# Kernel tuning notes

Measured on AMD Instinct MI355X. Metric: run time of the kernel, lower is better.

The kernel has to match this reference:

```python
import jax, jax.numpy as jnp
import numpy as np

TEMPERATURE = 0.1
CANTOR_WEIGHT = 0.3
P_POS = 256
GRID = 16
DIM = 512


def _cantor_bias():
    # matches LearnedWormholeRouter._compute_cantor_fingerprints / _compute_cantor_bias
    idx = np.arange(P_POS)
    x = idx % GRID
    y = idx // GRID
    s = x + y
    z = (s * (s + 1) // 2 + y).astype(np.float32)
    fp = z / max(z.max(), 1.0)
    aff = 1.0 - np.abs(fp[None, :] - fp[:, None])
    np.fill_diagonal(aff, -1e9)
    return (aff * CANTOR_WEIGHT).astype(np.float32)


def setup_inputs() -> dict:
    key = jax.random.key(0)
    ks = jax.random.split(key, 8)
    B, P, D = 64, P_POS, DIM
    sc = 0.02
    inp = {
        "x": jax.random.normal(ks[0], (B, P + 1, D), jnp.float32),
        "wq_r": jax.random.normal(ks[1], (D, D), jnp.float32) * sc,
        "bq_r": jnp.zeros((D,), jnp.float32),
        "wk_r": jax.random.normal(ks[2], (D, D), jnp.float32) * sc,
        "bk_r": jnp.zeros((D,), jnp.float32),
        "pos_bias": jnp.asarray(_cantor_bias()),
        "wq": jax.random.normal(ks[3], (D, D), jnp.float32) * sc,
        "bq": jnp.zeros((D,), jnp.float32),
        "wk": jax.random.normal(ks[4], (D, D), jnp.float32) * sc,
        "bk": jnp.zeros((D,), jnp.float32),
        "wv": jax.random.normal(ks[5], (D, D), jnp.float32) * sc,
        "bv": jnp.zeros((D,), jnp.float32),
        "wo": jax.random.normal(ks[6], (D, D), jnp.float32) * sc,
        "bo": jnp.zeros((D,), jnp.float32),
        "num_wormholes": 8,
        "num_heads": 8,
    }
    return inp


def _l2norm(v):
    return v / jnp.sqrt(jnp.sum(v * v, axis=-1, keepdims=True) + 1e-12)


def _gather_wormhole_multihead(xh, routes):
    # xh: [B,H,P,d], routes: [B,P,K] -> [B,H,P,K,d]
    # gather along the position axis, shared routes across heads
    idx = routes[:, None, :, :, None]            # [B,1,P,K,1]
    src = xh[:, :, None, :, :]                   # [B,H,1,P,d]
    return jnp.take_along_axis(src, idx, axis=3)  # [B,H,P,K,d]


def reference(x, wq_r, bq_r, wk_r, bk_r, pos_bias,
              wq, bq, wk, bk, wv, bv, wo, bo,
              num_wormholes, num_heads):
    B, P1, D = x.shape
    P = P1 - 1
    K = num_wormholes
    H = num_heads
    d = D // H

    xp = x[:, 1:, :]  # drop CLS token, [B,P,D]

    # --- LearnedWormholeRouter ---
    q_r = _l2norm(xp @ wq_r + bq_r)
    k_r = _l2norm(xp @ wk_r + bk_r)
    scores = jnp.einsum("bpd,bqd->bpq", q_r, k_r) + pos_bias[None]
    diag = jnp.eye(P, dtype=bool)
    scores = jnp.where(diag[None], -1e9, scores)
    scores_scaled = scores / TEMPERATURE
    topk_scores, routes = jax.lax.top_k(scores_scaled, K)  # [B,P,K]

    # --- wormhole multi-head attention over gathered positions ---
    def heads(w, b):
        return (xp @ w + b).reshape(B, P, H, d).transpose(0, 2, 1, 3)  # [B,H,P,d]

    qh, kh, vh = heads(wq, bq), heads(wk, bk), heads(wv, bv)
    gk = _gather_wormhole_multihead(kh, routes)  # [B,H,P,K,d]
    gv = _gather_wormhole_multihead(vh, routes)  # [B,H,P,K,d]

    att = jnp.einsum("bhpd,bhpkd->bhpk", qh, gk) / jnp.sqrt(jnp.float32(d))
    att = jax.nn.softmax(att, axis=-1)
    ctx = jnp.einsum("bhpk,bhpkd->bhpd", att, gv)
    out = ctx.transpose(0, 2, 1, 3).reshape(B, P, D) @ wo + bo  # [B,P,D]
    return out
```

## Files before the change

kernel.cpp:

```cpp
#include <hip/hip_runtime.h>
#include <math.h>

constexpr int PB = 256;
constexpr int DD = 512;
constexpr int NB = 64;
constexpr int MROWS = NB * PB;

typedef __bf16 bf16x8 __attribute__((ext_vector_type(8)));
typedef float f32x4 __attribute__((ext_vector_type(4)));
typedef unsigned short us8 __attribute__((ext_vector_type(8)));

__device__ __forceinline__ unsigned short f2b(float f) {
  unsigned int u = __float_as_uint(f);
  u += 0x7FFFu + ((u >> 16) & 1u);
  return (unsigned short)(u >> 16);
}
__device__ __forceinline__ float b2f(unsigned short h) {
  return __uint_as_float(((unsigned int)h) << 16);
}

__device__ __forceinline__ void gload16(const void* g, const void* l) {
  __builtin_amdgcn_global_load_lds(
      (const __attribute__((address_space(1))) unsigned int*)(uintptr_t)g,
      (__attribute__((address_space(3))) unsigned int*)(unsigned int)(uintptr_t)l,
      16, 0, 0);
}

__global__ __launch_bounds__(256) void gemm_scores(
    const float* __restrict__ Q, const float* __restrict__ Kr,
    float* __restrict__ S)
{
  __shared__ float As[16][65];
  __shared__ float Bs[16][65];
  const int b = blockIdx.z;
  const int tid = threadIdx.x;
  const int tx = tid & 15, ty = tid >> 4;
  const int p0 = blockIdx.y * 64, q0 = blockIdx.x * 64;
  const float* Qb = Q + (long)b * PB * DD;
  const float* Kb = Kr + (long)b * PB * DD;
  const int a_r = tid >> 2, a_k = (tid & 3) << 2;
  const int b_n = tid & 63, b_k4 = (tid >> 6) << 2;
  float acc[4][4] = {};

  for (int k0 = 0; k0 < DD; k0 += 16) {
    float4 av = *(const float4*)(Qb + (long)(p0 + a_r) * DD + k0 + a_k);
    As[a_k + 0][a_r] = av.x;
    As[a_k + 1][a_r] = av.y;
    As[a_k + 2][a_r] = av.z;
    As[a_k + 3][a_r] = av.w;
    float4 bv = *(const float4*)(Kb + (long)(q0 + b_n) * DD + k0 + b_k4);
    Bs[b_k4 + 0][b_n] = bv.x;
    Bs[b_k4 + 1][b_n] = bv.y;
    Bs[b_k4 + 2][b_n] = bv.z;
    Bs[b_k4 + 3][b_n] = bv.w;
    __syncthreads();
#pragma unroll
    for (int kk = 0; kk < 16; ++kk) {
      float a[4], b2[4];
#pragma unroll
      for (int i = 0; i < 4; ++i) a[i] = As[kk][ty * 4 + i];
#pragma unroll
      for (int j = 0; j < 4; ++j) b2[j] = Bs[kk][tx * 4 + j];
#pragma unroll
      for (int i = 0; i < 4; ++i)
#pragma unroll
        for (int j = 0; j < 4; ++j)
          acc[i][j] = fmaf(a[i], b2[j], acc[i][j]);
    }
    __syncthreads();
  }

  float* Sb = S + (long)b * PB * PB;
#pragma unroll
  for (int i = 0; i < 4; ++i) {
    int p = p0 + ty * 4 + i;
    int q = q0 + tx * 4;
    float4 o = make_float4(acc[i][0], acc[i][1], acc[i][2], acc[i][3]);
    *(float4*)(Sb + (long)p * PB + q) = o;
  }
}

__global__ __launch_bounds__(256) void split_x(
    const float* __restrict__ x, unsigned short* __restrict__ hi,
    unsigned short* __restrict__ lo)
{
  size_t i = (size_t)blockIdx.x * 256 + threadIdx.x;
  int row = (int)(i >> 6);
  int col = ((int)i & 63) << 3;
  const float* src = x + ((size_t)(row >> 8) * 257 + (row & 255) + 1) * DD + col;
  float4 a = *(const float4*)src;
  float4 b = *(const float4*)(src + 4);
  float v[8] = {a.x, a.y, a.z, a.w, b.x, b.y, b.z, b.w};
  us8 H, L;
#pragma unroll
  for (int j = 0; j < 8; ++j) {
    unsigned short h = f2b(v[j]);
    H[j] = h;
    L[j] = f2b(v[j] - b2f(h));
  }
  size_t o = (size_t)row * DD + col;
  *(us8*)(hi + o) = H;
  *(us8*)(lo + o) = L;
}

__global__ __launch_bounds__(256) void split_w(
    const float* __restrict__ W, unsigned short* __restrict__ hiT,
    unsigned short* __restrict__ loT)
{
  __shared__ float T[64][65];
  const int t = threadIdx.x;
  const int r0 = blockIdx.y * 64, c0 = blockIdx.x * 64;
  const int lr = t >> 2, lc4 = (t & 3) << 4;
#pragma unroll
  for (int j = 0; j < 4; ++j) {
    float4 v = *(const float4*)(W + (size_t)(r0 + lr) * DD + c0 + lc4 + j * 4);
    T[lr][lc4 + j * 4 + 0] = v.x;
    T[lr][lc4 + j * 4 + 1] = v.y;
    T[lr][lc4 + j * 4 + 2] = v.z;
    T[lr][lc4 + j * 4 + 3] = v.w;
  }
  __syncthreads();
  us8 H0, L0, H1, L1;
#pragma unroll
  for (int j = 0; j < 8; ++j) {
    float v0 = T[lc4 + j][lr];
    float v1 = T[lc4 + 8 + j][lr];
    unsigned short h0 = f2b(v0), h1 = f2b(v1);
    H0[j] = h0; L0[j] = f2b(v0 - b2f(h0));
    H1[j] = h1; L1[j] = f2b(v1 - b2f(h1));
  }
  size_t o = (size_t)(c0 + lr) * DD + r0 + lc4;
  *(us8*)(hiT + o) = H0;
  *(us8*)(hiT + o + 8) = H1;
  *(us8*)(loT + o) = L0;
  *(us8*)(loT + o + 8) = L1;
}

template<int NW>
__global__ __launch_bounds__(256) void gemm3m(
    const unsigned short* __restrict__ Ahi, const unsigned short* __restrict__ Alo,
    const unsigned short* __restrict__ B0h, const unsigned short* __restrict__ B0l,
    const unsigned short* __restrict__ B1h, const unsigned short* __restrict__ B1l,
    const unsigned short* __restrict__ B2h, const unsigned short* __restrict__ B2l,
    const float* __restrict__ bias0, const float* __restrict__ bias1,
    const float* __restrict__ bias2,
    float* __restrict__ C0, float* __restrict__ C1, float* __restrict__ C2)
{
  __shared__ unsigned short Ah[128 * 32], Al[128 * 32];
  __shared__ unsigned short Bh[128 * 32], Bl[128 * 32];
  const int tid = threadIdx.x;
  const int wave = tid >> 6, lane = tid & 63;
  const int wr = wave >> 1, wc = wave & 1;

  const int lid = blockIdx.y * (4 * NW) + blockIdx.x;
  const int swz = (lid & 7) * (64 * NW) + (lid >> 3);
  const int wsel = swz >> 9;
  const int r9 = swz & 511;
  const int row0 = (r9 >> 2) * 128, col0 = (r9 & 3) * 128;

  const unsigned short* BhiT = (NW == 1 || wsel == 0) ? B0h : (wsel == 1) ? B1h : B2h;
  const unsigned short* BloT = (NW == 1 || wsel == 0) ? B0l : (wsel == 1) ? B1l : B2l;
  const float* bias          = (NW == 1 || wsel == 0) ? bias0 : (wsel == 1) ? bias1 : bias2;
  float* C                   = (NW == 1 || wsel == 0) ? C0 : (wsel == 1) ? C1 : C2;

  const int lr = lane & 15, lk = lane >> 4;
  f32x4 acc[4][4] = {};

  const int sr = tid >> 2;
  const int schunk = (tid & 3) ^ ((sr >> 1) & 3);
  const unsigned int lds0 = (unsigned int)wave * 512;
  const size_t ga0 = (size_t)(row0 + sr) * DD + (schunk << 3);
  const size_t ga1 = ga0 + (size_t)64 * DD;
  const size_t gb0 = (size_t)(col0 + sr) * DD + (schunk << 3);
  const size_t gb1 = gb0 + (size_t)64 * DD;

  int aoff[4], boff[4];
#pragma unroll
  for (int m = 0; m < 4; ++m) {
    int row = wr * 64 + m * 16 + lr;
    aoff[m] = row * 32 + ((lk ^ ((row >> 1) & 3)) << 3);
  }
#pragma unroll
  for (int n = 0; n < 4; ++n) {
    int row = wc * 64 + n * 16 + lr;
    boff[n] = row * 32 + ((lk ^ ((row >> 1) & 3)) << 3);
  }

  for (int k0 = 0; k0 < DD; k0 += 32) {
    gload16(Ahi + ga0 + k0, Ah + lds0);
    gload16(Ahi + ga1 + k0, Ah + lds0 + 2048);
    gload16(Alo + ga0 + k0, Al + lds0);
    gload16(Alo + ga1 + k0, Al + lds0 + 2048);
    gload16(BhiT + gb0 + k0, Bh + lds0);
    gload16(BhiT + gb1 + k0, Bh + lds0 + 2048);
    gload16(BloT + gb0 + k0, Bl + lds0);
    gload16(BloT + gb1 + k0, Bl + lds0 + 2048);
    __syncthreads();

    bf16x8 a[8], b[8];
#pragma unroll
    for (int m = 0; m < 4; ++m) {
      a[m]     = *(const bf16x8*)(Ah + aoff[m]);
      a[m + 4] = *(const bf16x8*)(Al + aoff[m]);
    }
#pragma unroll
    for (int n = 0; n < 4; ++n) {
      b[n]     = *(const bf16x8*)(Bh + boff[n]);
      b[n + 4] = *(const bf16x8*)(Bl + boff[n]);
    }
#pragma unroll
    for (int m = 0; m < 4; ++m)
#pragma unroll
      for (int n = 0; n < 4; ++n) {
        f32x4 c = acc[m][n];
        c = __builtin_amdgcn_mfma_f32_16x16x32_bf16(a[m],     b[n],     c, 0, 0, 0);
        c = __builtin_amdgcn_mfma_f32_16x16x32_bf16(a[m],     b[n + 4], c, 0, 0, 0);
        c = __builtin_amdgcn_mfma_f32_16x16x32_bf16(a[m + 4], b[n],     c, 0, 0, 0);
        acc[m][n] = c;
      }
    __syncthreads();
  }

  float bcol[4];
#pragma unroll
  for (int n = 0; n < 4; ++n) bcol[n] = bias[col0 + wc * 64 + n * 16 + lr];
#pragma unroll
  for (int m = 0; m < 4; ++m)
#pragma unroll
    for (int j = 0; j < 4; ++j) {
      int r = row0 + wr * 64 + m * 16 + lk * 4 + j;
#pragma unroll
      for (int n = 0; n < 4; ++n)
        C[(size_t)r * DD + col0 + wc * 64 + n * 16 + lr] = acc[m][n][j] + bcol[n];
    }
}

__global__ __launch_bounds__(256) void l2norm_rows(float* __restrict__ X)
{
  const int row = blockIdx.x * 4 + (threadIdx.x >> 6);
  const int lane = threadIdx.x & 63;
  float* base = X + (long)row * DD + lane * 8;
  float4 u = *(float4*)base;
  float4 w = *(float4*)(base + 4);
  float s = u.x * u.x + u.y * u.y + u.z * u.z + u.w * u.w +
            w.x * w.x + w.y * w.y + w.z * w.z + w.w * w.w;
#pragma unroll
  for (int off = 1; off < 64; off <<= 1) s += __shfl_xor(s, off);
  float inv = 1.0f / sqrtf(s + 1e-12f);
  u.x *= inv; u.y *= inv; u.z *= inv; u.w *= inv;
  w.x *= inv; w.y *= inv; w.z *= inv; w.w *= inv;
  *(float4*)base = u;
  *(float4*)(base + 4) = w;
}

__global__ __launch_bounds__(256) void topk_routes(
    const float* __restrict__ S, const float* __restrict__ pb,
    int* __restrict__ routes)
{
  const int row = blockIdx.x * 4 + (threadIdx.x >> 6);
  const int lane = threadIdx.x & 63;
  const int p = row & 255;
  const float* srow = S + (long)row * 256;
  float v[4];
  int id[4];
#pragma unroll
  for (int i = 0; i < 4; ++i) {
    int q = i * 64 + lane;
    float s = srow[q] + pb[p * 256 + q];
    if (q == p) s = -1e9f;
    v[i] = s;
    id[i] = q;
  }
  for (int t = 0; t < 8; ++t) {
    float bv = v[0]; int bi = id[0]; int bs = 0;
#pragma unroll
    for (int i = 1; i < 4; ++i)
      if (v[i] > bv || (v[i] == bv && id[i] < bi)) { bv = v[i]; bi = id[i]; bs = i; }
    float rv = bv; int ri = bi;
#pragma unroll
    for (int off = 1; off < 64; off <<= 1) {
      float ov = __shfl_xor(rv, off);
      int oi = __shfl_xor(ri, off);
      if (ov > rv || (ov == rv && oi < ri)) { rv = ov; ri = oi; }
    }
    if (bi == ri) v[bs] = -INFINITY;
    if (lane == 0) routes[row * 8 + t] = ri;
  }
}

__global__ __launch_bounds__(512) void wormhole_attn(
    const float* __restrict__ qh, const float* __restrict__ kh,
    const float* __restrict__ vh, const int* __restrict__ routes,
    unsigned short* __restrict__ chi, unsigned short* __restrict__ clo)
{
  const int bp = blockIdx.x;
  const int b = bp >> 8;
  const int tid = threadIdx.x;
  __shared__ int rs[8];
  if (tid < 8) rs[tid] = routes[bp * 8 + tid];
  __syncthreads();

  const float q = qh[(long)bp * DD + tid];
  long rbase[8];
  float s[8];
#pragma unroll
  for (int k = 0; k < 8; ++k) {
    long roff = ((long)((b << 8) | rs[k])) * DD + tid;
    rbase[k] = roff;
    float t = q * kh[roff];
#pragma unroll
    for (int off = 1; off < 64; off <<= 1) t += __shfl_xor(t, off);
    s[k] = t * 0.125f;
  }
  float m = s[0];
#pragma unroll
  for (int k = 1; k < 8; ++k) m = fmaxf(m, s[k]);
  float e[8], sum = 0.f;
#pragma unroll
  for (int k = 0; k < 8; ++k) { e[k] = expf(s[k] - m); sum += e[k]; }
  float inv = 1.0f / sum;
  float c = 0.f;
#pragma unroll
  for (int k = 0; k < 8; ++k) c = fmaf(e[k] * inv, vh[rbase[k]], c);
  unsigned short h = f2b(c);
  chi[(size_t)bp * DD + tid] = h;
  clo[(size_t)bp * DD + tid] = f2b(c - b2f(h));
}

extern "C" void kernel_launch(void* const* d_in, const int* in_sizes, int n_in,
                              void* d_out, int out_size, void* d_ws, size_t ws_size,
                              hipStream_t stream)
{
  const float* x        = (const float*)d_in[0];
  const float* wq_r     = (const float*)d_in[1];
  const float* bq_r     = (const float*)d_in[2];
  const float* wk_r     = (const float*)d_in[3];
  const float* bk_r     = (const float*)d_in[4];
  const float* pos_bias = (const float*)d_in[5];
  const float* wq       = (const float*)d_in[6];
  const float* bq       = (const float*)d_in[7];
  const float* wk       = (const float*)d_in[8];
  const float* bk       = (const float*)d_in[9];
  const float* wv       = (const float*)d_in[10];
  const float* bv       = (const float*)d_in[11];
  const float* wo       = (const float*)d_in[12];
  const float* bo       = (const float*)d_in[13];

  char* w = (char*)d_ws;
  const size_t SLOT = (size_t)MROWS * DD * sizeof(float);
  unsigned short* Xhi = (unsigned short*)w;
  unsigned short* Xlo = (unsigned short*)(w + SLOT / 2);
  float* S0 = (float*)(w + SLOT);
  float* S1 = (float*)(w + 2 * SLOT);
  float* S2 = (float*)(w + 3 * SLOT);
  int* routes = (int*)(w + 4 * SLOT);
  const size_t WSZ = (size_t)DD * DD * sizeof(unsigned short);
  unsigned short* Wp = (unsigned short*)(w + 4 * SLOT + (1 << 20));
  unsigned short* Wq_hi = Wp + 0 * (WSZ / 2), *Wq_lo = Wp + 1 * (WSZ / 2);
  unsigned short* Wk_hi = Wp + 2 * (WSZ / 2), *Wk_lo = Wp + 3 * (WSZ / 2);
  unsigned short* Wv_hi = Wp + 4 * (WSZ / 2), *Wv_lo = Wp + 5 * (WSZ / 2);
  unsigned short* Wo_hi = Wp + 6 * (WSZ / 2), *Wo_lo = Wp + 7 * (WSZ / 2);

  unsigned short* Wr = (unsigned short*)(w + 3 * SLOT + SLOT / 2);
  unsigned short* Wqr_hi = Wr + 0 * (WSZ / 2), *Wqr_lo = Wr + 1 * (WSZ / 2);
  unsigned short* Wkr_hi = Wr + 2 * (WSZ / 2), *Wkr_lo = Wr + 3 * (WSZ / 2);

  unsigned short* Chi = Xhi;
  unsigned short* Clo = Xlo;

  dim3 blk(256);
  dim3 gw(8, 8);
  dim3 gs(4, 4, 64);
  dim3 g3r(8, 128);
  dim3 g3a(12, 128);
  dim3 g3b(4, 128);

  split_x<<<4096, 256, 0, stream>>>(x, Xhi, Xlo);
  split_w<<<gw, 256, 0, stream>>>(wq_r, Wqr_hi, Wqr_lo);
  split_w<<<gw, 256, 0, stream>>>(wk_r, Wkr_hi, Wkr_lo);
  split_w<<<gw, 256, 0, stream>>>(wq, Wq_hi, Wq_lo);
  split_w<<<gw, 256, 0, stream>>>(wk, Wk_hi, Wk_lo);
  split_w<<<gw, 256, 0, stream>>>(wv, Wv_hi, Wv_lo);
  split_w<<<gw, 256, 0, stream>>>(wo, Wo_hi, Wo_lo);

  gemm3m<2><<<g3r, blk, 0, stream>>>(Xhi, Xlo,
      Wqr_hi, Wqr_lo, Wkr_hi, Wkr_lo, Wkr_hi, Wkr_lo,
      bq_r, bk_r, bk_r, S0, S1, S1);
  l2norm_rows<<<(2 * MROWS) / 4, 256, 0, stream>>>(S0);
  gemm_scores<<<gs, blk, 0, stream>>>(S0, S1, S2);
  topk_routes<<<MROWS / 4, 256, 0, stream>>>(S2, pos_bias, routes);

  gemm3m<3><<<g3a, blk, 0, stream>>>(Xhi, Xlo,
      Wq_hi, Wq_lo, Wk_hi, Wk_lo, Wv_hi, Wv_lo,
      bq, bk, bv, S0, S1, S2);

  wormhole_attn<<<MROWS, 512, 0, stream>>>(S0, S1, S2, routes, Chi, Clo);
  gemm3m<1><<<g3b, blk, 0, stream>>>(Chi, Clo,
      Wo_hi, Wo_lo, Wo_hi, Wo_lo, Wo_hi, Wo_lo,
      bo, bo, bo, (float*)d_out, (float*)d_out, (float*)d_out);
}
```

Baseline: 522.9 us.

## Compute routing score GEMM with split-bf16 MFMA and fuse l2norm with bf16 split

```diff
diff --git a/kernel.cpp b/kernel.cpp
--- a/kernel.cpp
+++ b/kernel.cpp
@@ -24,60 +24,6 @@
       (const __attribute__((address_space(1))) unsigned int*)(uintptr_t)g,
       (__attribute__((address_space(3))) unsigned int*)(unsigned int)(uintptr_t)l,
       16, 0, 0);
-}
-
-__global__ __launch_bounds__(256) void gemm_scores(
-    const float* __restrict__ Q, const float* __restrict__ Kr,
-    float* __restrict__ S)
-{
-  __shared__ float As[16][65];
-  __shared__ float Bs[16][65];
-  const int b = blockIdx.z;
-  const int tid = threadIdx.x;
-  const int tx = tid & 15, ty = tid >> 4;
-  const int p0 = blockIdx.y * 64, q0 = blockIdx.x * 64;
-  const float* Qb = Q + (long)b * PB * DD;
-  const float* Kb = Kr + (long)b * PB * DD;
-  const int a_r = tid >> 2, a_k = (tid & 3) << 2;
-  const int b_n = tid & 63, b_k4 = (tid >> 6) << 2;
-  float acc[4][4] = {};
-
-  for (int k0 = 0; k0 < DD; k0 += 16) {
-    float4 av = *(const float4*)(Qb + (long)(p0 + a_r) * DD + k0 + a_k);
-    As[a_k + 0][a_r] = av.x;
-    As[a_k + 1][a_r] = av.y;
-    As[a_k + 2][a_r] = av.z;
-    As[a_k + 3][a_r] = av.w;
-    float4 bv = *(const float4*)(Kb + (long)(q0 + b_n) * DD + k0 + b_k4);
-    Bs[b_k4 + 0][b_n] = bv.x;
-    Bs[b_k4 + 1][b_n] = bv.y;
-    Bs[b_k4 + 2][b_n] = bv.z;
-    Bs[b_k4 + 3][b_n] = bv.w;
-    __syncthreads();
-#pragma unroll
-    for (int kk = 0; kk < 16; ++kk) {
-      float a[4], b2[4];
-#pragma unroll
-      for (int i = 0; i < 4; ++i) a[i] = As[kk][ty * 4 + i];
-#pragma unroll
-      for (int j = 0; j < 4; ++j) b2[j] = Bs[kk][tx * 4 + j];
-#pragma unroll
-      for (int i = 0; i < 4; ++i)
-#pragma unroll
-        for (int j = 0; j < 4; ++j)
-          acc[i][j] = fmaf(a[i], b2[j], acc[i][j]);
-    }
-    __syncthreads();
-  }
-
-  float* Sb = S + (long)b * PB * PB;
-#pragma unroll
-  for (int i = 0; i < 4; ++i) {
-    int p = p0 + ty * 4 + i;
-    int q = q0 + tx * 4;
-    float4 o = make_float4(acc[i][0], acc[i][1], acc[i][2], acc[i][3]);
-    *(float4*)(Sb + (long)p * PB + q) = o;
-  }
 }
 
 __global__ __launch_bounds__(256) void split_x(
@@ -235,22 +181,121 @@
     }
 }
 
-__global__ __launch_bounds__(256) void l2norm_rows(float* __restrict__ X)
+__global__ __launch_bounds__(256) void gemm3s(
+    const unsigned short* __restrict__ Qhi, const unsigned short* __restrict__ Qlo,
+    const unsigned short* __restrict__ Khi, const unsigned short* __restrict__ Klo,
+    float* __restrict__ S)
+{
+  __shared__ unsigned short Ah[128 * 32], Al[128 * 32];
+  __shared__ unsigned short Bh[128 * 32], Bl[128 * 32];
+  const int tid = threadIdx.x;
+  const int wave = tid >> 6, lane = tid & 63;
+  const int wr = wave >> 1, wc = wave & 1;
+
+  const int lid = blockIdx.z * 4 + blockIdx.y * 2 + blockIdx.x;
+  const int swz = (lid & 7) * 32 + (lid >> 3);
+  const int b = swz >> 2, t4 = swz & 3;
+  const int prow0 = b * PB + (t4 >> 1) * 128;
+  const int qrow0 = b * PB + (t4 & 1) * 128;
+
+  const int lr = lane & 15, lk = lane >> 4;
+  f32x4 acc[4][4] = {};
+
+  const int sr = tid >> 2;
+  const int schunk = (tid & 3) ^ ((sr >> 1) & 3);
+  const unsigned int lds0 = (unsigned int)wave * 512;
+  const size_t ga0 = (size_t)(prow0 + sr) * DD + (schunk << 3);
+  const size_t ga1 = ga0 + (size_t)64 * DD;
+  const size_t gb0 = (size_t)(qrow0 + sr) * DD + (schunk << 3);
+  const size_t gb1 = gb0 + (size_t)64 * DD;
+
+  int aoff[4], boff[4];
+#pragma unroll
+  for (int m = 0; m < 4; ++m) {
+    int row = wr * 64 + m * 16 + lr;
+    aoff[m] = row * 32 + ((lk ^ ((row >> 1) & 3)) << 3);
+  }
+#pragma unroll
+  for (int n = 0; n < 4; ++n) {
+    int row = wc * 64 + n * 16 + lr;
+    boff[n] = row * 32 + ((lk ^ ((row >> 1) & 3)) << 3);
+  }
+
+  for (int k0 = 0; k0 < DD; k0 += 32) {
+    gload16(Qhi + ga0 + k0, Ah + lds0);
+    gload16(Qhi + ga1 + k0, Ah + lds0 + 2048);
+    gload16(Qlo + ga0 + k0, Al + lds0);
+    gload16(Qlo + ga1 + k0, Al + lds0 + 2048);
+    gload16(Khi + gb0 + k0, Bh + lds0);
+    gload16(Khi + gb1 + k0, Bh + lds0 + 2048);
+    gload16(Klo + gb0 + k0, Bl + lds0);
+    gload16(Klo + gb1 + k0, Bl + lds0 + 2048);
+    __syncthreads();
+
+    bf16x8 a[8], bb[8];
+#pragma unroll
+    for (int m = 0; m < 4; ++m) {
+      a[m]     = *(const bf16x8*)(Ah + aoff[m]);
+      a[m + 4] = *(const bf16x8*)(Al + aoff[m]);
+    }
+#pragma unroll
+    for (int n = 0; n < 4; ++n) {
+      bb[n]     = *(const bf16x8*)(Bh + boff[n]);
+      bb[n + 4] = *(const bf16x8*)(Bl + boff[n]);
+    }
+#pragma unroll
+    for (int m = 0; m < 4; ++m)
+#pragma unroll
+      for (int n = 0; n < 4; ++n) {
+        f32x4 c = acc[m][n];
+        c = __builtin_amdgcn_mfma_f32_16x16x32_bf16(a[m],     bb[n],     c, 0, 0, 0);
+        c = __builtin_amdgcn_mfma_f32_16x16x32_bf16(a[m],     bb[n + 4], c, 0, 0, 0);
+        c = __builtin_amdgcn_mfma_f32_16x16x32_bf16(a[m + 4], bb[n],     c, 0, 0, 0);
+        acc[m][n] = c;
+      }
+    __syncthreads();
+  }
+
+  float* Sb = S + (size_t)b * PB * PB;
+#pragma unroll
+  for (int m = 0; m < 4; ++m)
+#pragma unroll
+    for (int j = 0; j < 4; ++j) {
+      int lp = (t4 >> 1) * 128 + wr * 64 + m * 16 + lk * 4 + j;
+#pragma unroll
+      for (int n = 0; n < 4; ++n) {
+        int lq = (t4 & 1) * 128 + wc * 64 + n * 16 + lr;
+        Sb[(size_t)lp * PB + lq] = acc[m][n][j];
+      }
+    }
+}
+
+__global__ __launch_bounds__(256) void l2norm_split(
+    const float* __restrict__ X, unsigned short* __restrict__ hi,
+    unsigned short* __restrict__ lo)
 {
   const int row = blockIdx.x * 4 + (threadIdx.x >> 6);
   const int lane = threadIdx.x & 63;
-  float* base = X + (long)row * DD + lane * 8;
-  float4 u = *(float4*)base;
-  float4 w = *(float4*)(base + 4);
+  const float* base = X + (size_t)row * DD + lane * 8;
+  float4 u = *(const float4*)base;
+  float4 w = *(const float4*)(base + 4);
   float s = u.x * u.x + u.y * u.y + u.z * u.z + u.w * u.w +
             w.x * w.x + w.y * w.y + w.z * w.z + w.w * w.w;
 #pragma unroll
   for (int off = 1; off < 64; off <<= 1) s += __shfl_xor(s, off);
   float inv = 1.0f / sqrtf(s + 1e-12f);
-  u.x *= inv; u.y *= inv; u.z *= inv; u.w *= inv;
-  w.x *= inv; w.y *= inv; w.z *= inv; w.w *= inv;
-  *(float4*)base = u;
-  *(float4*)(base + 4) = w;
+  float v[8] = {u.x * inv, u.y * inv, u.z * inv, u.w * inv,
+                w.x * inv, w.y * inv, w.z * inv, w.w * inv};
+  us8 H, L;
+#pragma unroll
+  for (int j = 0; j < 8; ++j) {
+    unsigned short h = f2b(v[j]);
+    H[j] = h;
+    L[j] = f2b(v[j] - b2f(h));
+  }
+  size_t o = (size_t)row * DD + lane * 8;
+  *(us8*)(hi + o) = H;
+  *(us8*)(lo + o) = L;
 }
 
 __global__ __launch_bounds__(256) void topk_routes(
@@ -348,32 +393,39 @@
 
   char* w = (char*)d_ws;
   const size_t SLOT = (size_t)MROWS * DD * sizeof(float);
+  const size_t PL   = (size_t)DD * DD;
+
   unsigned short* Xhi = (unsigned short*)w;
   unsigned short* Xlo = (unsigned short*)(w + SLOT / 2);
-  float* S0 = (float*)(w + SLOT);
-  float* S1 = (float*)(w + 2 * SLOT);
-  float* S2 = (float*)(w + 3 * SLOT);
+  float* P2 = (float*)(w + SLOT);
+  float* P3 = (float*)(w + 2 * SLOT);
+  char* s4 = w + 3 * SLOT;
+  unsigned short* Wqr_hi = (unsigned short*)s4;
+  unsigned short* Wqr_lo = Wqr_hi + PL;
+  unsigned short* Wkr_hi = Wqr_hi + 2 * PL;
+  unsigned short* Wkr_lo = Wqr_hi + 3 * PL;
+  unsigned short* Qr_hi = (unsigned short*)s4;
+  unsigned short* Qr_lo = (unsigned short*)(s4 + SLOT / 2);
+  unsigned short* Kr_hi = (unsigned short*)(w + SLOT);
+  unsigned short* Kr_lo = (unsigned short*)(w + SLOT + SLOT / 2);
+  float* Sc = P3;
+
   int* routes = (int*)(w + 4 * SLOT);
-  const size_t WSZ = (size_t)DD * DD * sizeof(unsigned short);
   unsigned short* Wp = (unsigned short*)(w + 4 * SLOT + (1 << 20));
-  unsigned short* Wq_hi = Wp + 0 * (WSZ / 2), *Wq_lo = Wp + 1 * (WSZ / 2);
-  unsigned short* Wk_hi = Wp + 2 * (WSZ / 2), *Wk_lo = Wp + 3 * (WSZ / 2);
-  unsigned short* Wv_hi = Wp + 4 * (WSZ / 2), *Wv_lo = Wp + 5 * (WSZ / 2);
-  unsigned short* Wo_hi = Wp + 6 * (WSZ / 2), *Wo_lo = Wp + 7 * (WSZ / 2);
-
-  unsigned short* Wr = (unsigned short*)(w + 3 * SLOT + SLOT / 2);
-  unsigned short* Wqr_hi = Wr + 0 * (WSZ / 2), *Wqr_lo = Wr + 1 * (WSZ / 2);
-  unsigned short* Wkr_hi = Wr + 2 * (WSZ / 2), *Wkr_lo = Wr + 3 * (WSZ / 2);
+  unsigned short* Wq_hi = Wp + 0 * PL, *Wq_lo = Wp + 1 * PL;
+  unsigned short* Wk_hi = Wp + 2 * PL, *Wk_lo = Wp + 3 * PL;
+  unsigned short* Wv_hi = Wp + 4 * PL, *Wv_lo = Wp + 5 * PL;
+  unsigned short* Wo_hi = Wp + 6 * PL, *Wo_lo = Wp + 7 * PL;
 
   unsigned short* Chi = Xhi;
   unsigned short* Clo = Xlo;
 
   dim3 blk(256);
   dim3 gw(8, 8);
-  dim3 gs(4, 4, 64);
   dim3 g3r(8, 128);
   dim3 g3a(12, 128);
   dim3 g3b(4, 128);
+  dim3 g3s(2, 2, 64);
 
   split_x<<<4096, 256, 0, stream>>>(x, Xhi, Xlo);
   split_w<<<gw, 256, 0, stream>>>(wq_r, Wqr_hi, Wqr_lo);
@@ -385,16 +437,19 @@
 
   gemm3m<2><<<g3r, blk, 0, stream>>>(Xhi, Xlo,
       Wqr_hi, Wqr_lo, Wkr_hi, Wkr_lo, Wkr_hi, Wkr_lo,
-      bq_r, bk_r, bk_r, S0, S1, S1);
-  l2norm_rows<<<(2 * MROWS) / 4, 256, 0, stream>>>(S0);
-  gemm_scores<<<gs, blk, 0, stream>>>(S0, S1, S2);
-  topk_routes<<<MROWS / 4, 256, 0, stream>>>(S2, pos_bias, routes);
+      bq_r, bk_r, bk_r, P2, P3, P3);
+
+  l2norm_split<<<MROWS / 4, 256, 0, stream>>>(P2, Qr_hi, Qr_lo);
+  l2norm_split<<<MROWS / 4, 256, 0, stream>>>(P3, Kr_hi, Kr_lo);
+
+  gemm3s<<<g3s, blk, 0, stream>>>(Qr_hi, Qr_lo, Kr_hi, Kr_lo, Sc);
+  topk_routes<<<MROWS / 4, 256, 0, stream>>>(Sc, pos_bias, routes);
 
   gemm3m<3><<<g3a, blk, 0, stream>>>(Xhi, Xlo,
       Wq_hi, Wq_lo, Wk_hi, Wk_lo, Wv_hi, Wv_lo,
-      bq, bk, bv, S0, S1, S2);
-
-  wormhole_attn<<<MROWS, 512, 0, stream>>>(S0, S1, S2, routes, Chi, Clo);
+      bq, bk, bv, (float*)s4, P2, P3);
+
+  wormhole_attn<<<MROWS, 512, 0, stream>>>((float*)s4, P2, P3, routes, Chi, Clo);
   gemm3m<1><<<g3b, blk, 0, stream>>>(Chi, Clo,
       Wo_hi, Wo_lo, Wo_hi, Wo_lo, Wo_hi, Wo_lo,
       bo, bo, bo, (float*)d_out, (float*)d_out, (float*)d_out);
```

Result: faster. 443.2 us (-15.2%).
